# Performance work log

Measured on AMD Instinct MI355X. Metric: run time of the kernel, lower is better.

The kernel has to match this reference:

```python
import jax, jax.numpy as jnp
import numpy as np

B, S, HID = 2, 2048, 2560
H, HKV, D = 8, 4, 256          # query heads, kv heads, head_dim
GROUPS = H // HKV
Q_SIZE, KV_SIZE = H * D, HKV * D
SLIDING_WINDOW = 512
SCALE = 256.0 ** -0.5          # query_pre_attn_scalar ** -0.5
EPS = 1e-6
ROPE_THETA = 10000.0


def setup_inputs() -> dict:
    key = jax.random.key(0)
    k1, k2, k3 = jax.random.split(key, 3)
    return {
        "hidden_states": jax.random.normal(k1, (B, S, HID), jnp.float32),
        "w_qkv": jax.random.normal(k2, (HID, Q_SIZE + 2 * KV_SIZE), jnp.float32) * (HID ** -0.5),
        "w_o": jax.random.normal(k3, (H * D, HID), jnp.float32) * ((H * D) ** -0.5),
        "q_norm_w": jnp.zeros((D,), jnp.float32),   # Gemma RMSNorm uses (1 + w)
        "k_norm_w": jnp.zeros((D,), jnp.float32),
        "positions": jnp.arange(S, dtype=jnp.int32),
    }


def _gemma_rms_norm(x, w, eps=EPS):
    # Gemma3RMSNorm: normalize in fp32, scale by (1 + w)
    xf = x.astype(jnp.float32)
    n = xf * jax.lax.rsqrt(jnp.mean(xf * xf, axis=-1, keepdims=True) + eps)
    return (n * (1.0 + w)).astype(x.dtype)


def _rope(q, k, positions):
    # q: [B,S,H,D], k: [B,S,HKV,D]; rotate_half RoPE, unsqueeze_dim=2 (head axis)
    half = D // 2
    inv_freq = 1.0 / (ROPE_THETA ** (jnp.arange(0, D, 2, dtype=jnp.float32) / D))  # [D/2]
    ang = positions.astype(jnp.float32)[:, None] * inv_freq[None, :]               # [S,D/2]
    emb = jnp.concatenate([ang, ang], axis=-1)                                     # [S,D]
    cos = jnp.cos(emb)[None, :, None, :]
    sin = jnp.sin(emb)[None, :, None, :]

    def rot(x):
        x1, x2 = x[..., :half], x[..., half:]
        return jnp.concatenate([-x2, x1], axis=-1)

    return q * cos + rot(q) * sin, k * cos + rot(k) * sin


def reference(hidden_states, w_qkv, w_o, q_norm_w, k_norm_w, positions):
    bsz, q_len, _ = hidden_states.shape
    qkv = jnp.einsum("bsh,hd->bsd", hidden_states, w_qkv)
    q, k, v = jnp.split(qkv, [Q_SIZE, Q_SIZE + KV_SIZE], axis=-1)
    Q = q.reshape(bsz, q_len, H, D)
    K = k.reshape(bsz, q_len, HKV, D)
    V = v.reshape(bsz, q_len, HKV, D)

    Q = _gemma_rms_norm(Q, q_norm_w)
    K = _gemma_rms_norm(K, k_norm_w)
    Q, K = _rope(Q, K, positions)

    # GQA: repeat kv heads to match query heads
    Kr = jnp.repeat(K, GROUPS, axis=2)  # [B,S,H,D]
    Vr = jnp.repeat(V, GROUPS, axis=2)

    scores = jnp.einsum("bqhd,bkhd->bhqk", Q, Kr) * SCALE  # [B,H,S,S]

    i = positions[:, None].astype(jnp.int32)
    j = positions[None, :].astype(jnp.int32)
    mask = (j <= i) & ((i - j) < SLIDING_WINDOW)           # causal + sliding window
    scores = jnp.where(mask[None, None, :, :], scores, jnp.float32(-1e30))

    probs = jax.nn.softmax(scores.astype(jnp.float32), axis=-1).astype(Q.dtype)
    out = jnp.einsum("bhqk,bkhd->bqhd", probs, Vr).reshape(bsz, q_len, H * D)
    return jnp.einsum("bsd,dh->bsh", out, w_o)
```

## Files before the change

### kernel.cpp

```cpp
#include <hip/hip_runtime.h>
#include <hip/hip_bf16.h>
#include <stdint.h>

#define QSCALE 0.09016844005555459f

typedef __attribute__((ext_vector_type(4))) float f32x4;
typedef __attribute__((ext_vector_type(8))) __bf16 bf16x8;
typedef __attribute__((ext_vector_type(8))) unsigned short ushort8;

static __device__ __forceinline__ float bf2f(unsigned short v) {
  union { unsigned u; float f; } x; x.u = ((unsigned)v) << 16; return x.f;
}
static __device__ __forceinline__ unsigned short f2bf(float f) {
  union { float f; unsigned u; } x; x.f = f;
  unsigned r = x.u + 0x7fffu + ((x.u >> 16) & 1u);
  return (unsigned short)(r >> 16);
}
static __device__ __forceinline__ void gload16(const void* g, void* l) {
  __builtin_amdgcn_global_load_lds((const __attribute__((address_space(1))) void*)g,
                                   (__attribute__((address_space(3))) void*)l, 16, 0, 0);
}
#define SBAR() __builtin_amdgcn_s_barrier()

__global__ __launch_bounds__(256) void k_rope_tab(const int* __restrict__ pos,
                                                  float* __restrict__ ct,
                                                  float* __restrict__ st) {
  int idx = blockIdx.x * 256 + threadIdx.x;
  int s = idx >> 7, j = idx & 127;
  float inv = exp2f((float)j * (-13.287712379549449f / 128.0f));
  float ang = (float)pos[s] * inv;
  float sv, cv;
  sincosf(ang, &sv, &cv);
  ct[idx] = cv; st[idx] = sv;
}

__global__ __launch_bounds__(256) void k_cvt_bf16(const float* __restrict__ in,
                                                  unsigned short* __restrict__ out, int n4) {
  int i = blockIdx.x * 256 + threadIdx.x;
  if (i >= n4) return;
  float4 v = ((const float4*)in)[i];
  ushort4 o; o.x = f2bf(v.x); o.y = f2bf(v.y); o.z = f2bf(v.z); o.w = f2bf(v.w);
  ((ushort4*)out)[i] = o;
}

__global__ __launch_bounds__(256) void k_transpose_w(const float* __restrict__ in,
                                                     unsigned short* __restrict__ out,
                                                     int R, int C) {
  __shared__ float tile[32][33];
  int c0 = blockIdx.x * 32, r0 = blockIdx.y * 32;
  int tx = threadIdx.x & 31, ty = threadIdx.x >> 5;
#pragma unroll
  for (int i = 0; i < 4; i++)
    tile[ty + 8*i][tx] = in[(size_t)(r0 + ty + 8*i) * C + c0 + tx];
  __syncthreads();
#pragma unroll
  for (int i = 0; i < 4; i++)
    out[(size_t)(c0 + ty + 8*i) * R + r0 + tx] = f2bf(tile[tx][ty + 8*i]);
}

template <bool F32OUT>
__global__ __launch_bounds__(512, 1) void k_gemm256(const unsigned short* __restrict__ A,
                                                    const unsigned short* __restrict__ Bt,
                                                    void* __restrict__ Cm,
                                                    int M, int N, int K) {
  __shared__ __align__(16) unsigned short ldsA[4][8192];
  __shared__ __align__(16) unsigned short ldsB[4][8192];
  const int nbn = N >> 8;
  int bid = blockIdx.x;
  int nwg = gridDim.x;
  if ((nwg & 7) == 0) {
    int cpx = nwg >> 3;
    bid = (bid & 7) * cpx + (bid >> 3);
  }
  const int bm = bid / nbn, bn = bid % nbn;
  const int tid = threadIdx.x;
  const int w = tid >> 6, l = tid & 63;
  const int wm = w >> 2, wn = w & 3;
  const int lr = l & 15, lk = l >> 4;
  const int nt = K >> 5;

  const int rL = tid >> 2;
  const int swc = ((tid & 3) ^ ((tid >> 3) & 3)) << 3;
  const unsigned short* Ag = A + (size_t)(bm * 256 + rL) * K + swc;
  const unsigned short* Bg = Bt + (size_t)(bn * 256 + rL) * K + swc;
  const int ldsoff = w * 512;
  const int wb = ((lk ^ ((lr >> 1) & 3)) << 3);
  const int arow0 = wm * 128 + lr;
  const int brow0 = wn * 64 + lr;

  f32x4 acc[8][4] = {};

#define STAGE_A(kt_, s_) do { \
    gload16(Ag + (size_t)(kt_) * 32,                    (char*)&ldsA[s_][ldsoff]); \
    gload16(Ag + (size_t)(kt_) * 32 + (size_t)128 * K,  (char*)&ldsA[s_][4096 + ldsoff]); } while (0)
#define STAGE_B(kt_, s_) do { \
    gload16(Bg + (size_t)(kt_) * 32,                    (char*)&ldsB[s_][ldsoff]); \
    gload16(Bg + (size_t)(kt_) * 32 + (size_t)128 * K,  (char*)&ldsB[s_][4096 + ldsoff]); } while (0)

#define KSTEP(kt_, S_, PF_, VMC_, TAILBAR_) do { \
    bf16x8 af[8], bf[4]; \
    _Pragma("unroll") \
    for (int i = 0; i < 8; ++i) \
      af[i] = *(const bf16x8*)&ldsA[S_][((arow0 + i * 16) << 5) + wb]; \
    _Pragma("unroll") \
    for (int j = 0; j < 4; ++j) \
      bf[j] = *(const bf16x8*)&ldsB[S_][((brow0 + j * 16) << 5) + wb]; \
    if (PF_) { STAGE_A((kt_) + 3, ((S_) + 3) & 3); STAGE_B((kt_) + 3, ((S_) + 3) & 3); } \
    __builtin_amdgcn_s_setprio(1); \
    _Pragma("unroll") \
    for (int i = 0; i < 8; ++i) \
      _Pragma("unroll") \
      for (int j = 0; j < 4; ++j) \
        acc[i][j] = __builtin_amdgcn_mfma_f32_16x16x32_bf16(af[i], bf[j], acc[i][j], 0, 0, 0); \
    __builtin_amdgcn_s_setprio(0); \
    if ((VMC_) == 8)      { asm volatile("s_waitcnt vmcnt(8)" ::: "memory"); } \
    else if ((VMC_) == 4) { asm volatile("s_waitcnt vmcnt(4)" ::: "memory"); } \
    else if ((VMC_) == 0) { asm volatile("s_waitcnt vmcnt(0)" ::: "memory"); } \
    if (TAILBAR_) SBAR(); \
  } while (0)

  STAGE_A(0, 0); STAGE_B(0, 0);
  STAGE_A(1, 1); STAGE_B(1, 1);
  STAGE_A(2, 2); STAGE_B(2, 2);
  asm volatile("s_waitcnt vmcnt(8)" ::: "memory");
  SBAR();

  const int ng = nt >> 2;
  for (int g = 0; g < ng - 1; ++g) {
    const int kt0 = g << 2;
    KSTEP(kt0 + 0, 0, true, 8, true);
    KSTEP(kt0 + 1, 1, true, 8, true);
    KSTEP(kt0 + 2, 2, true, 8, true);
    KSTEP(kt0 + 3, 3, true, 8, true);
  }
  {
    const int kt0 = nt - 4;
    KSTEP(kt0 + 0, 0, true, 8, true);
    KSTEP(kt0 + 1, 1, false, 4, true);
    KSTEP(kt0 + 2, 2, false, 0, true);
    KSTEP(kt0 + 3, 3, false, -1, false);
  }
#undef KSTEP
#undef STAGE_A
#undef STAGE_B

#pragma unroll
  for (int i = 0; i < 8; ++i)
#pragma unroll
    for (int j = 0; j < 4; ++j) {
      int row = bm * 256 + wm * 128 + i * 16 + lk * 4;
      int col = bn * 256 + wn * 64 + j * 16 + lr;
#pragma unroll
      for (int r = 0; r < 4; ++r) {
        if constexpr (F32OUT)
          ((float*)Cm)[(size_t)(row + r) * N + col] = acc[i][j][r];
        else
          ((unsigned short*)Cm)[(size_t)(row + r) * N + col] = f2bf(acc[i][j][r]);
      }
    }
}

__global__ __launch_bounds__(256) void k_norm_rope(
    const unsigned short* __restrict__ qkv,
    const float* __restrict__ qw, const float* __restrict__ kw,
    const float* __restrict__ ct, const float* __restrict__ st,
    unsigned short* __restrict__ Qh, unsigned short* __restrict__ Kh) {
  int gwid = (blockIdx.x * 256 + threadIdx.x) >> 6;
  int l = threadIdx.x & 63;
  int head = gwid % 12;
  int bs = gwid / 12;
  int b = bs >> 11, s = bs & 2047;
  bool isq = head < 8;
  int col = isq ? head * 256 : 2048 + (head - 8) * 256;
  const unsigned short* src = qkv + (size_t)bs * 4096 + col;
  int d0 = l * 4;
  ushort4 u = *(const ushort4*)(src + d0);
  float x0 = bf2f(u.x), x1 = bf2f(u.y), x2 = bf2f(u.z), x3 = bf2f(u.w);
  float ss = x0 * x0 + x1 * x1 + x2 * x2 + x3 * x3;
#pragma unroll
  for (int off = 32; off > 0; off >>= 1) ss += __shfl_xor(ss, off);
  float inv = rsqrtf(ss * (1.0f / 256.0f) + 1e-6f);
  const float* wv = isq ? qw : kw;
  float4 w4 = *(const float4*)(wv + d0);
  float y0 = x0 * inv * (1.0f + w4.x);
  float y1 = x1 * inv * (1.0f + w4.y);
  float y2 = x2 * inv * (1.0f + w4.z);
  float y3 = x3 * inv * (1.0f + w4.w);
  int fb = (l & 31) * 4;
  float4 c4 = *(const float4*)(ct + s * 128 + fb);
  float4 s4 = *(const float4*)(st + s * 128 + fb);
  float p0 = __shfl_xor(y0, 32), p1 = __shfl_xor(y1, 32);
  float p2 = __shfl_xor(y2, 32), p3 = __shfl_xor(y3, 32);
  float sg = (l < 32) ? -1.0f : 1.0f;
  float o0 = y0 * c4.x + sg * p0 * s4.x;
  float o1 = y1 * c4.y + sg * p1 * s4.y;
  float o2 = y2 * c4.z + sg * p2 * s4.z;
  float o3 = y3 * c4.w + sg * p3 * s4.w;
  if (isq) {
    o0 *= QSCALE; o1 *= QSCALE; o2 *= QSCALE; o3 *= QSCALE;
    unsigned short* dst = Qh + (((size_t)(b * 8 + head)) * 2048 + s) * 256 + d0;
    ushort4 o; o.x = f2bf(o0); o.y = f2bf(o1); o.z = f2bf(o2); o.w = f2bf(o3);
    *(ushort4*)dst = o;
  } else {
    int hk = head - 8;
    int ch = d0 >> 3;
    int dsw = ((ch ^ (s & 7)) << 3) | (d0 & 7);
    unsigned short* dst = Kh + (((size_t)(b * 4 + hk)) * 2048 + s) * 256 + dsw;
    ushort4 o; o.x = f2bf(o0); o.y = f2bf(o1); o.z = f2bf(o2); o.w = f2bf(o3);
    *(ushort4*)dst = o;
  }
}

__global__ __launch_bounds__(256) void k_vtrans(const unsigned short* __restrict__ qkv,
                                                unsigned short* __restrict__ VT) {
  __shared__ __align__(16) unsigned short tile[64][72];
  int bid = blockIdx.x;
  int dt = bid & 3, stile = (bid >> 2) & 31, hk = (bid >> 7) & 3, b = bid >> 9;
  int s0 = stile * 64, d0 = dt * 64;
  int t = threadIdx.x;
#pragma unroll
  for (int i = 0; i < 2; i++) {
    int flat = i * 256 + t;
    int sl = flat >> 3, dc = flat & 7;
    ushort8 v = *(const ushort8*)&qkv[(size_t)(b * 2048 + s0 + sl) * 4096 + 3072 + hk * 256 + d0 + dc * 8];
    *(ushort8*)&tile[sl][dc * 8] = v;
  }
  __syncthreads();
#pragma unroll
  for (int i = 0; i < 2; i++) {
    int flat = i * 256 + t;
    int dl = flat >> 3, sc = flat & 7;
    ushort8 v;
#pragma unroll
    for (int j = 0; j < 8; j++) v[j] = tile[sc * 8 + j][dl];
    int dg = d0 + dl;
    int chg = (s0 >> 3) + sc;
    int swc = chg ^ (dg & 7);
    *(ushort8*)&VT[((size_t)(b * 4 + hk) * 256 + dg) * 2048 + swc * 8] = v;
  }
}

__global__ __launch_bounds__(256) void k_attn(
    const unsigned short* __restrict__ Qh,
    const unsigned short* __restrict__ Kh,
    const unsigned short* __restrict__ VT,
    const int* __restrict__ pos,
    unsigned short* __restrict__ Ao) {
  __shared__ __align__(16) unsigned short Ks[64 * 256];
  __shared__ __align__(16) unsigned short Vs[256 * 64];
  __shared__ __align__(16) unsigned short Ps[4][16 * 72];
  int bid = blockIdx.x;
  int qt = bid & 31, h = (bid >> 5) & 7, b = bid >> 8;
  int hk = h >> 1;
  int t = threadIdx.x, w = t >> 6, l = t & 63;
  int lr = l & 15, lk = l >> 4;
  int q0 = qt * 64, qrow0 = q0 + w * 16;
  const unsigned short* qbase = Qh + (((size_t)(b * 8 + h)) * 2048 + (qrow0 + lr)) * 256;
  bf16x8 qf[8];
#pragma unroll
  for (int c = 0; c < 8; c++) qf[c] = *(const bf16x8*)&qbase[c * 32 + lk * 8];
  int pq[4];
#pragma unroll
  for (int r = 0; r < 4; r++) pq[r] = pos[qrow0 + lk * 4 + r];
  float m[4], ll[4];
  f32x4 oacc[16];
  f32x4 zero4 = {0.f, 0.f, 0.f, 0.f};
#pragma unroll
  for (int r = 0; r < 4; r++) { m[r] = -1e30f; ll[r] = 0.0f; }
#pragma unroll
  for (int nd = 0; nd < 16; nd++) oacc[nd] = zero4;
  const char* Kbase = (const char*)(Kh + ((size_t)(b * 4 + hk)) * 2048 * 256);
  const char* Vbase = (const char*)(VT + ((size_t)(b * 4 + hk)) * 256 * 2048);
  int jlo = q0 - 511; if (jlo < 0) jlo = 0; jlo &= ~63;
  for (int j0 = jlo; j0 < q0 + 64; j0 += 64) {
#pragma unroll
    for (int i = 0; i < 8; i++)
      gload16(Kbase + (size_t)j0 * 512 + i * 4096 + t * 16, (char*)Ks + i * 4096 + w * 1024);
#pragma unroll
    for (int i = 0; i < 8; i++) {
      int off = i * 4096 + t * 16;
      int d = off >> 7, rb = off & 127;
      gload16(Vbase + (size_t)d * 4096 + j0 * 2 + rb, (char*)Vs + i * 4096 + w * 1024);
    }
    __syncthreads();
    f32x4 sacc[4];
#pragma unroll
    for (int n = 0; n < 4; n++) sacc[n] = zero4;
#pragma unroll
    for (int n = 0; n < 4; n++) {
      int key = n * 16 + lr;
      int sw = (key & 7) << 4;
#pragma unroll
      for (int c = 0; c < 8; c++) {
        bf16x8 kf = *(const bf16x8*)((const char*)Ks + key * 512 + ((c * 64 + lk * 16) ^ sw));
        sacc[n] = __builtin_amdgcn_mfma_f32_16x16x32_bf16(qf[c], kf, sacc[n], 0, 0, 0);
      }
    }
    int pk[4];
#pragma unroll
    for (int n = 0; n < 4; n++) pk[n] = pos[j0 + n * 16 + lr];
#pragma unroll
    for (int n = 0; n < 4; n++)
#pragma unroll
      for (int r = 0; r < 4; r++) {
        int dq = pq[r] - pk[n];
        if (!(dq >= 0 && dq < 512)) sacc[n][r] = -1e30f;
      }
    float tm[4], rs[4], mn[4], corr[4];
#pragma unroll
    for (int r = 0; r < 4; r++)
      tm[r] = fmaxf(fmaxf(sacc[0][r], sacc[1][r]), fmaxf(sacc[2][r], sacc[3][r]));
#pragma unroll
    for (int d = 1; d < 16; d <<= 1)
#pragma unroll
      for (int r = 0; r < 4; r++) tm[r] = fmaxf(tm[r], __shfl_xor(tm[r], d));
#pragma unroll
    for (int r = 0; r < 4; r++) {
      mn[r] = fmaxf(m[r], tm[r]);
      corr[r] = exp2f(m[r] - mn[r]);
      rs[r] = 0.f;
    }
#pragma unroll
    for (int n = 0; n < 4; n++)
#pragma unroll
      for (int r = 0; r < 4; r++) {
        float sv = sacc[n][r];
        float p = (sv > -1e29f) ? exp2f(sv - mn[r]) : 0.0f;
        sacc[n][r] = p;
        rs[r] += p;
      }
#pragma unroll
    for (int d = 1; d < 16; d <<= 1)
#pragma unroll
      for (int r = 0; r < 4; r++) rs[r] += __shfl_xor(rs[r], d);
#pragma unroll
    for (int r = 0; r < 4; r++) { ll[r] = ll[r] * corr[r] + rs[r]; m[r] = mn[r]; }
#pragma unroll
    for (int nd = 0; nd < 16; nd++)
#pragma unroll
      for (int r = 0; r < 4; r++) oacc[nd][r] *= corr[r];
#pragma unroll
    for (int n = 0; n < 4; n++)
#pragma unroll
      for (int r = 0; r < 4; r++)
        Ps[w][(lk * 4 + r) * 72 + n * 16 + lr] = f2bf(sacc[n][r]);
#pragma unroll
    for (int c2 = 0; c2 < 2; c2++) {
      bf16x8 pf = *(const bf16x8*)&Ps[w][lr * 72 + c2 * 32 + lk * 8];
#pragma unroll
      for (int nd = 0; nd < 16; nd++) {
        int dr = nd * 16 + lr;
        bf16x8 vf = *(const bf16x8*)((const char*)Vs + dr * 128 + ((c2 * 64 + lk * 16) ^ ((dr & 7) << 4)));
        oacc[nd] = __builtin_amdgcn_mfma_f32_16x16x32_bf16(pf, vf, oacc[nd], 0, 0, 0);
      }
    }
    __syncthreads();
  }
#pragma unroll
  for (int r = 0; r < 4; r++) ll[r] = 1.0f / ll[r];
#pragma unroll
  for (int nd = 0; nd < 16; nd++)
#pragma unroll
    for (int r = 0; r < 4; r++) {
      float v = oacc[nd][r] * ll[r];
      Ao[((size_t)(b * 2048 + qrow0 + lk * 4 + r)) * 2048 + h * 256 + nd * 16 + lr] = f2bf(v);
    }
}

extern "C" void kernel_launch(void* const* d_in, const int* in_sizes, int n_in,
                              void* d_out, int out_size, void* d_ws, size_t ws_size,
                              hipStream_t stream) {
  const float* hs   = (const float*)d_in[0];
  const float* wqkv = (const float*)d_in[1];
  const float* wo   = (const float*)d_in[2];
  const float* qnw  = (const float*)d_in[3];
  const float* knw  = (const float*)d_in[4];
  const int*   pos  = (const int*)d_in[5];
  float* out = (float*)d_out;

  char* base = (char*)d_ws;
  const size_t OFF_R0 = 0;
  const size_t OFF_R1 = 33554432;
  const size_t OFF_R2 = 54525952;
  const size_t OFF_R3 = 75497472;

  unsigned short* QKV = (unsigned short*)(base + OFF_R0);
  unsigned short* Ao  = (unsigned short*)(base + OFF_R0);
  unsigned short* WoT = (unsigned short*)(base + OFF_R0 + 16777216);
  unsigned short* Xb  = (unsigned short*)(base + OFF_R1);
  unsigned short* Qh  = (unsigned short*)(base + OFF_R1);
  unsigned short* WqT = (unsigned short*)(base + OFF_R2);
  unsigned short* Kh  = (unsigned short*)(base + OFF_R2);
  unsigned short* VT  = (unsigned short*)(base + OFF_R2 + 8388608);
  float* ct = (float*)(base + OFF_R3);
  float* st = (float*)(base + OFF_R3 + 1048576);

  k_rope_tab<<<1024, 256, 0, stream>>>(pos, ct, st);
  k_cvt_bf16<<<10240, 256, 0, stream>>>(hs, Xb, 2621440);
  k_transpose_w<<<dim3(128, 80), 256, 0, stream>>>(wqkv, WqT, 2560, 4096);
  k_gemm256<false><<<256, 512, 0, stream>>>(Xb, WqT, QKV, 4096, 4096, 2560);
  k_norm_rope<<<12288, 256, 0, stream>>>(QKV, qnw, knw, ct, st, Qh, Kh);
  k_vtrans<<<1024, 256, 0, stream>>>(QKV, VT);
  k_transpose_w<<<dim3(80, 64), 256, 0, stream>>>(wo, WoT, 2048, 2560);
  k_attn<<<512, 256, 0, stream>>>(Qh, Kh, VT, pos, Ao);
  k_gemm256<true><<<160, 512, 0, stream>>>(Ao, WoT, out, 4096, 2560, 2048);
}
```

Baseline: 251.4 us.

## Double-buffer GEMM LDS fragments in registers to overlap reads with MFMA

The bf16 GEMM main loop now reads the next k-step's A/B fragments from LDS into a second register set before issuing the current step's MFMAs. Before, each step's LDS reads sat directly ahead of its own MFMAs. Waitcnt values and the prologue and tail are adjusted so that stage kt+2 is resident one step earlier. This aims to hide LDS read latency behind matrix math. The cost is about 48 more VGPRs for the extra fragment set, and wait and barrier placement that is harder to get right.

```diff
diff --git a/kernel.cpp b/kernel.cpp
--- a/kernel.cpp
+++ b/kernel.cpp
@@ -89,6 +89,7 @@
   const int brow0 = wn * 64 + lr;
 
   f32x4 acc[8][4] = {};
+  bf16x8 afA[8], bfA[4], afB[8], bfB[4];
 
 #define STAGE_A(kt_, s_) do { \
     gload16(Ag + (size_t)(kt_) * 32,                    (char*)&ldsA[s_][ldsoff]); \
@@ -97,50 +98,54 @@
     gload16(Bg + (size_t)(kt_) * 32,                    (char*)&ldsB[s_][ldsoff]); \
     gload16(Bg + (size_t)(kt_) * 32 + (size_t)128 * K,  (char*)&ldsB[s_][4096 + ldsoff]); } while (0)
 
-#define KSTEP(kt_, S_, PF_, VMC_, TAILBAR_) do { \
-    bf16x8 af[8], bf[4]; \
+#define FRAG_READ(S_, AF_, BF_) do { \
     _Pragma("unroll") \
     for (int i = 0; i < 8; ++i) \
-      af[i] = *(const bf16x8*)&ldsA[S_][((arow0 + i * 16) << 5) + wb]; \
+      AF_[i] = *(const bf16x8*)&ldsA[S_][((arow0 + i * 16) << 5) + wb]; \
     _Pragma("unroll") \
     for (int j = 0; j < 4; ++j) \
-      bf[j] = *(const bf16x8*)&ldsB[S_][((brow0 + j * 16) << 5) + wb]; \
-    if (PF_) { STAGE_A((kt_) + 3, ((S_) + 3) & 3); STAGE_B((kt_) + 3, ((S_) + 3) & 3); } \
+      BF_[j] = *(const bf16x8*)&ldsB[S_][((brow0 + j * 16) << 5) + wb]; \
+  } while (0)
+
+#define KSTEP(kt_, SNXT_, PFR_, CURAF_, CURBF_, NXTAF_, NXTBF_, STG_, VMC_, BAR_) do { \
+    if (PFR_) FRAG_READ(SNXT_, NXTAF_, NXTBF_); \
+    if (STG_) { STAGE_A((kt_) + 3, ((kt_) + 3) & 3); STAGE_B((kt_) + 3, ((kt_) + 3) & 3); } \
     __builtin_amdgcn_s_setprio(1); \
     _Pragma("unroll") \
     for (int i = 0; i < 8; ++i) \
       _Pragma("unroll") \
       for (int j = 0; j < 4; ++j) \
-        acc[i][j] = __builtin_amdgcn_mfma_f32_16x16x32_bf16(af[i], bf[j], acc[i][j], 0, 0, 0); \
+        acc[i][j] = __builtin_amdgcn_mfma_f32_16x16x32_bf16(CURAF_[i], CURBF_[j], acc[i][j], 0, 0, 0); \
     __builtin_amdgcn_s_setprio(0); \
-    if ((VMC_) == 8)      { asm volatile("s_waitcnt vmcnt(8)" ::: "memory"); } \
-    else if ((VMC_) == 4) { asm volatile("s_waitcnt vmcnt(4)" ::: "memory"); } \
+    if ((VMC_) == 4)      { asm volatile("s_waitcnt vmcnt(4)" ::: "memory"); } \
     else if ((VMC_) == 0) { asm volatile("s_waitcnt vmcnt(0)" ::: "memory"); } \
-    if (TAILBAR_) SBAR(); \
+    if (BAR_) SBAR(); \
   } while (0)
 
   STAGE_A(0, 0); STAGE_B(0, 0);
   STAGE_A(1, 1); STAGE_B(1, 1);
   STAGE_A(2, 2); STAGE_B(2, 2);
-  asm volatile("s_waitcnt vmcnt(8)" ::: "memory");
+  asm volatile("s_waitcnt vmcnt(4)" ::: "memory");
   SBAR();
+  FRAG_READ(0, afA, bfA);
 
   const int ng = nt >> 2;
   for (int g = 0; g < ng - 1; ++g) {
     const int kt0 = g << 2;
-    KSTEP(kt0 + 0, 0, true, 8, true);
-    KSTEP(kt0 + 1, 1, true, 8, true);
-    KSTEP(kt0 + 2, 2, true, 8, true);
-    KSTEP(kt0 + 3, 3, true, 8, true);
+    KSTEP(kt0 + 0, 1, true, afA, bfA, afB, bfB, true, 4, true);
+    KSTEP(kt0 + 1, 2, true, afB, bfB, afA, bfA, true, 4, true);
+    KSTEP(kt0 + 2, 3, true, afA, bfA, afB, bfB, true, 4, true);
+    KSTEP(kt0 + 3, 0, true, afB, bfB, afA, bfA, true, 4, true);
   }
   {
     const int kt0 = nt - 4;
-    KSTEP(kt0 + 0, 0, true, 8, true);
-    KSTEP(kt0 + 1, 1, false, 4, true);
-    KSTEP(kt0 + 2, 2, false, 0, true);
-    KSTEP(kt0 + 3, 3, false, -1, false);
+    KSTEP(kt0 + 0, 1, true, afA, bfA, afB, bfB, true,  4, true);
+    KSTEP(kt0 + 1, 2, true, afB, bfB, afA, bfA, false, 0, true);
+    KSTEP(kt0 + 2, 3, true, afA, bfA, afB, bfB, false, -1, false);
+    KSTEP(kt0 + 3, 0, false, afB, bfB, afA, bfA, false, -1, false);
   }
 #undef KSTEP
+#undef FRAG_READ
 #undef STAGE_A
 #undef STAGE_B
 
```

Result: slower. 270.3 us (+7.5%).

## Restructure GEMM into double-buffered 64-wide K tiles with barrier-interleaved MFMA phases

Applied to the files above, without the earlier changes.

The 256x256 GEMM kernel now uses two LDS buffers of 64-wide K tiles instead of a four-stage ring of 32-wide tiles. Each tile is split into four sub-phases that read A fragments, then run MFMA, with barriers between phases in a ping-pong style. This halves the number of K iterations and aims to overlap LDS reads, global prefetch and MFMA work across waves. In exchange the prefetch depth drops to one tile ahead, there are many more barriers per tile, and vmcnt(0) waits could expose global memory latency.

```diff
diff --git a/kernel.cpp b/kernel.cpp
--- a/kernel.cpp
+++ b/kernel.cpp
@@ -59,12 +59,11 @@
 }
 
 template <bool F32OUT>
-__global__ __launch_bounds__(512, 1) void k_gemm256(const unsigned short* __restrict__ A,
-                                                    const unsigned short* __restrict__ Bt,
-                                                    void* __restrict__ Cm,
-                                                    int M, int N, int K) {
-  __shared__ __align__(16) unsigned short ldsA[4][8192];
-  __shared__ __align__(16) unsigned short ldsB[4][8192];
+__global__ __launch_bounds__(512, 1) void k_gemm8p(const unsigned short* __restrict__ A,
+                                                   const unsigned short* __restrict__ Bt,
+                                                   void* __restrict__ Cm,
+                                                   int M, int N, int K) {
+  __shared__ __align__(16) unsigned short lds[65536];
   const int nbn = N >> 8;
   int bid = blockIdx.x;
   int nwg = gridDim.x;
@@ -77,72 +76,89 @@
   const int w = tid >> 6, l = tid & 63;
   const int wm = w >> 2, wn = w & 3;
   const int lr = l & 15, lk = l >> 4;
-  const int nt = K >> 5;
-
-  const int rL = tid >> 2;
-  const int swc = ((tid & 3) ^ ((tid >> 3) & 3)) << 3;
-  const unsigned short* Ag = A + (size_t)(bm * 256 + rL) * K + swc;
-  const unsigned short* Bg = Bt + (size_t)(bn * 256 + rL) * K + swc;
-  const int ldsoff = w * 512;
+  const int nt = K >> 6;
+
+  const int srow = tid >> 2, schk = tid & 3;
+  const int gcx = ((schk ^ ((srow >> 1) & 3)) << 3);
+  const unsigned short* aS = A + (size_t)(bm * 256 + srow) * K + gcx;
+  const unsigned short* bS = Bt + (size_t)(bn * 256 + srow) * K + gcx;
   const int wb = ((lk ^ ((lr >> 1) & 3)) << 3);
-  const int arow0 = wm * 128 + lr;
-  const int brow0 = wn * 64 + lr;
 
   f32x4 acc[8][4] = {};
-
-#define STAGE_A(kt_, s_) do { \
-    gload16(Ag + (size_t)(kt_) * 32,                    (char*)&ldsA[s_][ldsoff]); \
-    gload16(Ag + (size_t)(kt_) * 32 + (size_t)128 * K,  (char*)&ldsA[s_][4096 + ldsoff]); } while (0)
-#define STAGE_B(kt_, s_) do { \
-    gload16(Bg + (size_t)(kt_) * 32,                    (char*)&ldsB[s_][ldsoff]); \
-    gload16(Bg + (size_t)(kt_) * 32 + (size_t)128 * K,  (char*)&ldsB[s_][4096 + ldsoff]); } while (0)
-
-#define KSTEP(kt_, S_, PF_, VMC_, TAILBAR_) do { \
-    bf16x8 af[8], bf[4]; \
+  bf16x8 af[2][2];
+  bf16x8 bf[4][2];
+
+#define STAGE_T(T_, DB_) do { \
+    const unsigned short* a0_ = aS + (size_t)(T_) * 64; \
+    const unsigned short* b0_ = bS + (size_t)(T_) * 64; \
+    const int d_ = (DB_) * 16384 + tid * 8; \
+    gload16(a0_,                       (char*)&lds[d_]); \
+    gload16(a0_ + 32,                  (char*)&lds[d_ + 4096]); \
+    gload16(a0_ + (size_t)128 * K,     (char*)&lds[d_ + 8192]); \
+    gload16(a0_ + (size_t)128 * K + 32,(char*)&lds[d_ + 12288]); \
+    gload16(b0_,                       (char*)&lds[32768 + d_]); \
+    gload16(b0_ + 32,                  (char*)&lds[32768 + d_ + 4096]); \
+    gload16(b0_ + (size_t)128 * K,     (char*)&lds[32768 + d_ + 8192]); \
+    gload16(b0_ + (size_t)128 * K + 32,(char*)&lds[32768 + d_ + 12288]); \
+  } while (0)
+
+#define RD_AF(S_, Q_) do { \
+    const int ab_ = (S_) * 16384 + wm * 8192; \
     _Pragma("unroll") \
-    for (int i = 0; i < 8; ++i) \
-      af[i] = *(const bf16x8*)&ldsA[S_][((arow0 + i * 16) << 5) + wb]; \
+    for (int kh = 0; kh < 2; ++kh) { \
+      af[0][kh] = *(const bf16x8*)&lds[ab_ + kh * 4096 + ((((Q_)*2+0)*16 + lr) << 5) + wb]; \
+      af[1][kh] = *(const bf16x8*)&lds[ab_ + kh * 4096 + ((((Q_)*2+1)*16 + lr) << 5) + wb]; \
+    } \
+  } while (0)
+
+#define RD_BF(S_) do { \
+    const int bb_ = 32768 + (S_) * 16384 + (wn >> 1) * 8192; \
     _Pragma("unroll") \
     for (int j = 0; j < 4; ++j) \
-      bf[j] = *(const bf16x8*)&ldsB[S_][((brow0 + j * 16) << 5) + wb]; \
-    if (PF_) { STAGE_A((kt_) + 3, ((S_) + 3) & 3); STAGE_B((kt_) + 3, ((S_) + 3) & 3); } \
+      _Pragma("unroll") \
+      for (int kh = 0; kh < 2; ++kh) \
+        bf[j][kh] = *(const bf16x8*)&lds[bb_ + kh * 4096 + (((wn & 1) * 64 + j * 16 + lr) << 5) + wb]; \
+  } while (0)
+
+#define MFMA_Q(Q_) do { \
     __builtin_amdgcn_s_setprio(1); \
     _Pragma("unroll") \
-    for (int i = 0; i < 8; ++i) \
+    for (int ii = 0; ii < 2; ++ii) \
       _Pragma("unroll") \
-      for (int j = 0; j < 4; ++j) \
-        acc[i][j] = __builtin_amdgcn_mfma_f32_16x16x32_bf16(af[i], bf[j], acc[i][j], 0, 0, 0); \
+      for (int j = 0; j < 4; ++j) { \
+        acc[(Q_)*2+ii][j] = __builtin_amdgcn_mfma_f32_16x16x32_bf16(af[ii][0], bf[j][0], acc[(Q_)*2+ii][j], 0, 0, 0); \
+        acc[(Q_)*2+ii][j] = __builtin_amdgcn_mfma_f32_16x16x32_bf16(af[ii][1], bf[j][1], acc[(Q_)*2+ii][j], 0, 0, 0); \
+      } \
     __builtin_amdgcn_s_setprio(0); \
-    if ((VMC_) == 8)      { asm volatile("s_waitcnt vmcnt(8)" ::: "memory"); } \
-    else if ((VMC_) == 4) { asm volatile("s_waitcnt vmcnt(4)" ::: "memory"); } \
-    else if ((VMC_) == 0) { asm volatile("s_waitcnt vmcnt(0)" ::: "memory"); } \
-    if (TAILBAR_) SBAR(); \
   } while (0)
 
-  STAGE_A(0, 0); STAGE_B(0, 0);
-  STAGE_A(1, 1); STAGE_B(1, 1);
-  STAGE_A(2, 2); STAGE_B(2, 2);
-  asm volatile("s_waitcnt vmcnt(8)" ::: "memory");
+#define TILE(T_, S_) do { \
+    const bool pf_ = (T_) + 1 < nt; \
+     \
+    RD_AF(S_, 0); RD_BF(S_); \
+    if (pf_) STAGE_T((T_) + 1, 1 - (S_)); \
+    SBAR(); MFMA_Q(0); SBAR(); \
+     RD_AF(S_, 1); SBAR(); MFMA_Q(1); SBAR(); \
+     RD_AF(S_, 2); SBAR(); MFMA_Q(2); SBAR(); \
+     \
+    RD_AF(S_, 3); \
+    asm volatile("s_waitcnt vmcnt(0)" ::: "memory"); \
+    SBAR(); MFMA_Q(3); SBAR(); \
+  } while (0)
+
+  STAGE_T(0, 0);
+  asm volatile("s_waitcnt vmcnt(0)" ::: "memory");
   SBAR();
 
-  const int ng = nt >> 2;
-  for (int g = 0; g < ng - 1; ++g) {
-    const int kt0 = g << 2;
-    KSTEP(kt0 + 0, 0, true, 8, true);
-    KSTEP(kt0 + 1, 1, true, 8, true);
-    KSTEP(kt0 + 2, 2, true, 8, true);
-    KSTEP(kt0 + 3, 3, true, 8, true);
-  }
-  {
-    const int kt0 = nt - 4;
-    KSTEP(kt0 + 0, 0, true, 8, true);
-    KSTEP(kt0 + 1, 1, false, 4, true);
-    KSTEP(kt0 + 2, 2, false, 0, true);
-    KSTEP(kt0 + 3, 3, false, -1, false);
-  }
-#undef KSTEP
-#undef STAGE_A
-#undef STAGE_B
+  for (int t = 0; t < nt; t += 2) {
+    TILE(t, 0);
+    TILE(t + 1, 1);
+  }
+#undef TILE
+#undef MFMA_Q
+#undef RD_BF
+#undef RD_AF
+#undef STAGE_T
 
 #pragma unroll
   for (int i = 0; i < 8; ++i)
@@ -398,10 +414,10 @@
   k_rope_tab<<<1024, 256, 0, stream>>>(pos, ct, st);
   k_cvt_bf16<<<10240, 256, 0, stream>>>(hs, Xb, 2621440);
   k_transpose_w<<<dim3(128, 80), 256, 0, stream>>>(wqkv, WqT, 2560, 4096);
-  k_gemm256<false><<<256, 512, 0, stream>>>(Xb, WqT, QKV, 4096, 4096, 2560);
+  k_gemm8p<false><<<256, 512, 0, stream>>>(Xb, WqT, QKV, 4096, 4096, 2560);
   k_norm_rope<<<12288, 256, 0, stream>>>(QKV, qnw, knw, ct, st, Qh, Kh);
   k_vtrans<<<1024, 256, 0, stream>>>(QKV, VT);
   k_transpose_w<<<dim3(80, 64), 256, 0, stream>>>(wo, WoT, 2048, 2560);
   k_attn<<<512, 256, 0, stream>>>(Qh, Kh, VT, pos, Ao);
-  k_gemm256<true><<<160, 512, 0, stream>>>(Ao, WoT, out, 4096, 2560, 2048);
-}
+  k_gemm8p<true><<<160, 512, 0, stream>>>(Ao, WoT, out, 4096, 2560, 2048);
+}
```

Result: slower. 262.5 us (+4.4%).
